# Performance work log

Measured on AMD Instinct MI355X. Metric: run time of the kernel, lower is better.

Reference implementation:

```python
import jax, jax.numpy as jnp
import numpy as np


def setup_inputs() -> dict:
    key = jax.random.key(0)
    k1, k2, k3, k4 = jax.random.split(key, 4)
    TOKENS, IN_F, OUT_F = 4096, 4096, 11008
    x = jax.random.normal(k1, (TOKENS, IN_F), dtype=jnp.float32)
    # int8-valued weights stored in fp32 buffer, as in the torch module
    quantized_weight = jax.random.randint(k2, (OUT_F, IN_F), -128, 128).astype(jnp.float32)
    # per-output-channel scales, positive, small (like max|w|/127)
    weight_scales = (jax.random.uniform(k3, (OUT_F, 1), dtype=jnp.float32) * 0.03 + 0.001)
    bias = jax.random.normal(k4, (OUT_F,), dtype=jnp.float32)
    return {"x": x, "quantized_weight": quantized_weight,
            "weight_scales": weight_scales, "bias": bias}


def reference(x, quantized_weight, weight_scales, bias):
    # dequantize: per-channel scale broadcast over in_features
    weight = quantized_weight * weight_scales  # [out, in]
    # F.linear: x @ weight.T + bias
    return jnp.dot(x, weight.T) + bias
```

## Files before the change

### kernel.cpp

```cpp
#include <hip/hip_runtime.h>
#include <hip/hip_bf16.h>


typedef __attribute__((ext_vector_type(4))) int   i32x4;
typedef __attribute__((ext_vector_type(4))) float f32x4;
typedef __attribute__((ext_vector_type(4))) unsigned int u32x4;

__device__ static inline unsigned int pack4(int q0, int q1, int q2, int q3) {
    return (unsigned)(q0 & 255) | ((unsigned)(q1 & 255) << 8) |
           ((unsigned)(q2 & 255) << 16) | ((unsigned)(q3 & 255) << 24);
}

__global__ void w_to_i8(const float* __restrict__ in,
                        u32x4* __restrict__ out, long n16) {
    const long stride = (long)gridDim.x * blockDim.x;
    for (long i = (long)blockIdx.x * blockDim.x + threadIdx.x; i < n16; i += stride) {
        const f32x4* p = reinterpret_cast<const f32x4*>(in) + i * 4;
        u32x4 o;
#pragma unroll
        for (int v = 0; v < 4; ++v) {
            f32x4 f = p[v];
            o[v] = pack4(__float2int_rn(f[0]), __float2int_rn(f[1]),
                         __float2int_rn(f[2]), __float2int_rn(f[3]));
        }
        out[i] = o;
    }
}

__global__ void x_quant_i8(const float* __restrict__ x,
                           unsigned int* __restrict__ xq,
                           float* __restrict__ sx, int K) {
    const int row = blockIdx.x;
    const int tid = threadIdx.x;
    const float* xr = x + (size_t)row * K;
    float m = 0.f;
    for (int b = tid * 16; b < K; b += blockDim.x * 16) {
        const f32x4* p = (const f32x4*)(xr + b);
#pragma unroll
        for (int v = 0; v < 4; ++v) {
            f32x4 f = p[v];
            m = fmaxf(m, fmaxf(fmaxf(fabsf(f[0]), fabsf(f[1])),
                               fmaxf(fabsf(f[2]), fabsf(f[3]))));
        }
    }
#pragma unroll
    for (int off = 32; off; off >>= 1) m = fmaxf(m, __shfl_xor(m, off));
    __shared__ float red[8];
    if ((tid & 63) == 0) red[tid >> 6] = m;
    __syncthreads();
    const int nw = blockDim.x >> 6;
    m = red[0];
    for (int i = 1; i < nw; ++i) m = fmaxf(m, red[i]);
    const float inv = (m > 0.f) ? 127.0f / m : 0.f;
    if (tid == 0) sx[row] = m * (1.0f / 127.0f);
    for (int b = tid * 16; b < K; b += blockDim.x * 16) {
        const f32x4* p = (const f32x4*)(xr + b);
        u32x4 o;
#pragma unroll
        for (int v = 0; v < 4; ++v) {
            f32x4 f = p[v];
            int q0 = min(127, max(-127, __float2int_rn(f[0] * inv)));
            int q1 = min(127, max(-127, __float2int_rn(f[1] * inv)));
            int q2 = min(127, max(-127, __float2int_rn(f[2] * inv)));
            int q3 = min(127, max(-127, __float2int_rn(f[3] * inv)));
            o[v] = pack4(q0, q1, q2, q3);
        }
        *reinterpret_cast<u32x4*>((char*)xq + (size_t)row * K + b) = o;
    }
}


#define GLOAD16(src, dst) __builtin_amdgcn_global_load_lds( \
    (const __attribute__((address_space(1))) void*)(src),   \
    (__attribute__((address_space(3))) void*)(dst), 16, 0, 0)

#define FENCE() asm volatile("" ::: "memory")
#define BAR()  do { FENCE(); __builtin_amdgcn_s_barrier(); FENCE(); } while (0)
#define WAIT_VM(n) asm volatile("s_waitcnt vmcnt(" #n ")" ::: "memory")
#define WAIT_LGKM0() asm volatile("s_waitcnt lgkmcnt(0)" ::: "memory")
#define PACE_LGKM(n) asm volatile("s_waitcnt lgkmcnt(" #n ")" ::: "memory")
#define SCHED0() __builtin_amdgcn_sched_barrier(0)

__global__ __launch_bounds__(512, 2)
void qlinear_gemm_i8k128(const char* __restrict__ A,
                         const char* __restrict__ B,
                         const float* __restrict__ sx,
                         const float* __restrict__ scales,
                         const float* __restrict__ bias,
                         float* __restrict__ C,
                         int M, int N, int K, int nbx) {
    __shared__ __align__(128) char smem[131072];

    const int tid  = threadIdx.x;
    const int lane = tid & 63;
    const int wid  = tid >> 6;
    const int wr   = wid >> 2;
    const int wc   = wid & 3;

    const int nwg = gridDim.x;
    const int q = nwg >> 3, r = nwg & 7;
    const int xcd = blockIdx.x & 7, boff_ = blockIdx.x >> 3;
    const int swz = (xcd < r ? xcd * (q + 1) : r * (q + 1) + (xcd - r) * q) + boff_;
    const int bcol = swz % nbx;
    const int brow = swz / nbx;

    const char* Ag = A + (size_t)brow * 256 * K;
    const char* Bg = B + (size_t)bcol * 256 * K;

    size_t sA[2], sB[2];
#pragma unroll
    for (int g = 0; g < 2; ++g) {
        const int c = tid + g * 512, rl = c >> 3, j = c & 7;
        const int rowA = ((rl >> 6) << 7) + (rl & 63);
        const int rowB = ((rl >> 5) << 6) + (rl & 31);
        sA[g] = (size_t)rowA * K + ((j ^ (rl & 7)) << 4);
        sB[g] = (size_t)rowB * K + ((j ^ (rl & 7)) << 4);
    }
    const int ld0 = tid * 16;

    auto stageA = [&](int rg, int h, int t) {
        const char* G = Ag + (size_t)h * 64 * K + (size_t)t * 128;
        char* base = smem + rg * 32768 + h * 16384;
        GLOAD16(G + sA[0], base + ld0);
        GLOAD16(G + sA[1], base + ld0 + 8192);
    };
    auto stageB = [&](int rg, int h, int t) {
        const char* G = Bg + (size_t)h * 32 * K + (size_t)t * 128;
        char* base = smem + 65536 + rg * 32768 + h * 16384;
        GLOAD16(G + sB[0], base + ld0);
        GLOAD16(G + sB[1], base + ld0 + 8192);
    };

    const int px0 = (((lane >> 4) ^ (lane & 7)) << 4);
    const int px1 = (((4 + (lane >> 4)) ^ (lane & 7)) << 4);
    const int arow = (wr * 64 + (lane & 15)) * 128;
    const int brw  = (wc * 32 + (lane & 15)) * 128;

    i32x4 acc[8][4] = {};
    i32x4 a0[8], a1[8], b0[4], b1[4];

    auto rdA = [&](int rg, int mh, i32x4 (&d)[8]) {
        const char* p = smem + rg * 32768 + mh * 16384 + arow;
#pragma unroll
        for (int i = 0; i < 4; ++i) {
            d[i * 2]     = *(const i32x4*)(p + i * 2048 + px0);
            d[i * 2 + 1] = *(const i32x4*)(p + i * 2048 + px1);
        }
    };
    auto rdB = [&](int rg, int nh, i32x4 (&d)[4]) {
        const char* p = smem + 65536 + rg * 32768 + nh * 16384 + brw;
#pragma unroll
        for (int n = 0; n < 2; ++n) {
            d[n * 2]     = *(const i32x4*)(p + n * 2048 + px0);
            d[n * 2 + 1] = *(const i32x4*)(p + n * 2048 + px1);
        }
    };
    auto mfma16 = [&](const i32x4 (&a)[8], const i32x4 (&b)[4], int mh, int nh) {
        __builtin_amdgcn_s_setprio(1);
#pragma unroll
        for (int i = 0; i < 4; ++i)
#pragma unroll
            for (int n = 0; n < 2; ++n) {
                i32x4& ac = acc[mh * 4 + i][nh * 2 + n];
                ac = __builtin_amdgcn_mfma_i32_16x16x64_i8(a[i * 2], b[n * 2], ac, 0, 0, 0);
                ac = __builtin_amdgcn_mfma_i32_16x16x64_i8(a[i * 2 + 1], b[n * 2 + 1], ac, 0, 0, 0);
            }
        __builtin_amdgcn_s_setprio(0);
    };

    const int NT = K / 128;

    stageA(0, 0, 0); stageB(0, 0, 0); stageA(0, 1, 0); stageB(0, 1, 0);
    stageA(1, 0, 1); stageB(1, 0, 1); stageA(1, 1, 1);
    WAIT_VM(6); BAR();

    for (int t = 0; t < NT - 2; ++t) {
        const int c = t & 1, o = c ^ 1;
        rdA(c, 0, a0); rdB(c, 0, b0);
        stageB(o, 1, t + 1);
        PACE_LGKM(8);
        BAR(); WAIT_LGKM0(); SCHED0();
        mfma16(a0, b0, 0, 0);
        BAR();
        rdA(c, 1, a1);
        stageA(c, 0, t + 2);
        BAR(); WAIT_LGKM0(); SCHED0();
        mfma16(a1, b0, 1, 0);
        BAR();
        rdB(c, 1, b1);
        stageB(c, 0, t + 2);
        BAR(); WAIT_LGKM0(); SCHED0();
        mfma16(a0, b1, 0, 1);
        BAR();
        stageA(c, 1, t + 2);
        mfma16(a1, b1, 1, 1);
        WAIT_VM(6);
        BAR();
    }
    {
        const int c = (NT - 2) & 1, o = c ^ 1;
        rdA(c, 0, a0); rdB(c, 0, b0);
        stageB(o, 1, NT - 1);
        PACE_LGKM(8);
        BAR(); WAIT_LGKM0(); SCHED0();
        mfma16(a0, b0, 0, 0);
        BAR();
        rdA(c, 1, a1);
        BAR(); WAIT_LGKM0(); SCHED0();
        mfma16(a1, b0, 1, 0);
        BAR();
        rdB(c, 1, b1);
        BAR(); WAIT_LGKM0(); SCHED0();
        mfma16(a0, b1, 0, 1);
        BAR();
        mfma16(a1, b1, 1, 1);
        WAIT_VM(0);
        BAR();
    }
    {
        const int c = (NT - 1) & 1;
        rdA(c, 0, a0); rdB(c, 0, b0);
        WAIT_LGKM0(); SCHED0();
        mfma16(a0, b0, 0, 0);
        rdA(c, 1, a1);
        WAIT_LGKM0(); SCHED0();
        mfma16(a1, b0, 1, 0);
        rdB(c, 1, b1);
        WAIT_LGKM0(); SCHED0();
        mfma16(a0, b1, 0, 1);
        mfma16(a1, b1, 1, 1);
    }

    const int lc  = lane & 15;
    const int lr4 = (lane >> 4) * 4;
    float sarr[4], barr[4];
#pragma unroll
    for (int ni = 0; ni < 4; ++ni) {
        const int n = bcol * 256 + wc * 64 + (ni >> 1) * 32 + (ni & 1) * 16 + lc;
        sarr[ni] = scales[n];
        barr[ni] = bias[n];
    }
#pragma unroll
    for (int mi = 0; mi < 8; ++mi) {
        const int mb = brow * 256 + wr * 128 + (mi >> 2) * 64 + (mi & 3) * 16 + lr4;
#pragma unroll
        for (int j = 0; j < 4; ++j) {
            const size_t rowoff = (size_t)(mb + j) * N;
            const float sm = sx[mb + j];
#pragma unroll
            for (int ni = 0; ni < 4; ++ni) {
                const int n = bcol * 256 + wc * 64 + (ni >> 1) * 32 + (ni & 1) * 16 + lc;
                C[rowoff + n] = fmaf((float)acc[mi][ni][j], sm * sarr[ni], barr[ni]);
            }
        }
    }
}

__global__ void qlinear_fallback(const float* __restrict__ A,
                                 const float* __restrict__ B,
                                 const float* __restrict__ scales,
                                 const float* __restrict__ bias,
                                 float* __restrict__ C, int M, int N, int K) {
    __shared__ float As[16][17], Bs[16][17];
    const int tx = threadIdx.x, ty = threadIdx.y;
    const int row = blockIdx.y * 16 + ty;
    const int col = blockIdx.x * 16 + tx;
    float acc = 0.f;
    for (int k0 = 0; k0 < K; k0 += 16) {
        As[ty][tx] = A[(long)row * K + k0 + tx];
        Bs[ty][tx] = B[(long)(blockIdx.x * 16 + ty) * K + k0 + tx];
        __syncthreads();
#pragma unroll
        for (int kk = 0; kk < 16; ++kk) acc += As[ty][kk] * Bs[tx][kk];
        __syncthreads();
    }
    C[(long)row * N + col] = fmaf(acc, scales[col], bias[col]);
}

extern "C" void kernel_launch(void* const* d_in, const int* in_sizes, int n_in,
                              void* d_out, int out_size, void* d_ws, size_t ws_size,
                              hipStream_t stream) {
    const float* x      = (const float*)d_in[0];
    const float* w      = (const float*)d_in[1];
    const float* scales = (const float*)d_in[2];
    const float* bias   = (const float*)d_in[3];
    float* out = (float*)d_out;

    const int N = in_sizes[2];
    const int K = (int)((long)in_sizes[1] / N);
    const int M = (int)((long)in_sizes[0] / K);

    const size_t need = (size_t)M * K + (size_t)N * K + (size_t)M * 4;
    const bool ok = (ws_size >= need) && (M % 256) == 0 && (N % 256) == 0 &&
                    (K % 128) == 0 && (K / 128) >= 3 && (K % 16) == 0;

    if (ok) {
        char* xq = (char*)d_ws;
        char* wq = xq + (size_t)M * K;
        float* sxbuf = (float*)(wq + (size_t)N * K);

        x_quant_i8<<<M, 256, 0, stream>>>(x, (unsigned int*)xq, sxbuf, K);
        w_to_i8<<<2048, 256, 0, stream>>>(w, (u32x4*)wq, (long)N * K / 16);

        const int nbx = N / 256;
        const int nwg = (M / 256) * nbx;
        qlinear_gemm_i8k128<<<nwg, 512, 0, stream>>>(xq, wq, sxbuf, scales, bias,
                                                     out, M, N, K, nbx);
    } else {
        dim3 grid(N / 16, M / 16), blk(16, 16);
        qlinear_fallback<<<grid, blk, 0, stream>>>(x, w, scales, bias, out, M, N, K);
    }
}
```

Before: 253.8 us.

## Restructure int8 GEMM main loop into two phases with fewer barriers

Reorganizes the K-loop from four barrier-separated MFMA quarters into two halves. Each half loads both B fragments (or the second A fragment) and issues two MFMA groups back-to-back. Global-to-LDS staging of the next tiles is regrouped so that A and B halves are issued together, and the prologue/wait counts are adjusted to match. This cuts barrier count per iteration and lengthens uninterrupted MFMA runs, at the cost of holding more fragment registers live at once. It also changes how far ahead prefetches are issued, which risks exposing load latency or LDS hazards.

```diff
diff --git a/kernel.cpp b/kernel.cpp
--- a/kernel.cpp
+++ b/kernel.cpp
@@ -78,17 +78,16 @@
 #define BAR()  do { FENCE(); __builtin_amdgcn_s_barrier(); FENCE(); } while (0)
 #define WAIT_VM(n) asm volatile("s_waitcnt vmcnt(" #n ")" ::: "memory")
 #define WAIT_LGKM0() asm volatile("s_waitcnt lgkmcnt(0)" ::: "memory")
-#define PACE_LGKM(n) asm volatile("s_waitcnt lgkmcnt(" #n ")" ::: "memory")
 #define SCHED0() __builtin_amdgcn_sched_barrier(0)
 
 __global__ __launch_bounds__(512, 2)
-void qlinear_gemm_i8k128(const char* __restrict__ A,
-                         const char* __restrict__ B,
-                         const float* __restrict__ sx,
-                         const float* __restrict__ scales,
-                         const float* __restrict__ bias,
-                         float* __restrict__ C,
-                         int M, int N, int K, int nbx) {
+void qlinear_gemm_i8v2(const char* __restrict__ A,
+                       const char* __restrict__ B,
+                       const float* __restrict__ sx,
+                       const float* __restrict__ scales,
+                       const float* __restrict__ bias,
+                       float* __restrict__ C,
+                       int M, int N, int K, int nbx) {
     __shared__ __align__(128) char smem[131072];
 
     const int tid  = threadIdx.x;
@@ -156,7 +155,6 @@
         }
     };
     auto mfma16 = [&](const i32x4 (&a)[8], const i32x4 (&b)[4], int mh, int nh) {
-        __builtin_amdgcn_s_setprio(1);
 #pragma unroll
         for (int i = 0; i < 4; ++i)
 #pragma unroll
@@ -165,69 +163,62 @@
                 ac = __builtin_amdgcn_mfma_i32_16x16x64_i8(a[i * 2], b[n * 2], ac, 0, 0, 0);
                 ac = __builtin_amdgcn_mfma_i32_16x16x64_i8(a[i * 2 + 1], b[n * 2 + 1], ac, 0, 0, 0);
             }
-        __builtin_amdgcn_s_setprio(0);
     };
 
     const int NT = K / 128;
 
     stageA(0, 0, 0); stageB(0, 0, 0); stageA(0, 1, 0); stageB(0, 1, 0);
-    stageA(1, 0, 1); stageB(1, 0, 1); stageA(1, 1, 1);
-    WAIT_VM(6); BAR();
+    stageA(1, 0, 1); stageB(1, 0, 1);
+    WAIT_VM(4); BAR();
 
     for (int t = 0; t < NT - 2; ++t) {
         const int c = t & 1, o = c ^ 1;
-        rdA(c, 0, a0); rdB(c, 0, b0);
-        stageB(o, 1, t + 1);
-        PACE_LGKM(8);
-        BAR(); WAIT_LGKM0(); SCHED0();
+        stageA(o, 1, t + 1); stageB(o, 1, t + 1);
+        rdA(c, 0, a0); rdB(c, 0, b0); rdB(c, 1, b1);
+        WAIT_LGKM0(); SCHED0();
+        __builtin_amdgcn_s_setprio(1);
         mfma16(a0, b0, 0, 0);
+        mfma16(a0, b1, 0, 1);
+        __builtin_amdgcn_s_setprio(0);
+        BAR();
+        stageA(c, 0, t + 2); stageB(c, 0, t + 2);
+        rdA(c, 1, a1);
+        WAIT_LGKM0(); SCHED0();
+        __builtin_amdgcn_s_setprio(1);
+        mfma16(a1, b0, 1, 0);
+        mfma16(a1, b1, 1, 1);
+        __builtin_amdgcn_s_setprio(0);
+        WAIT_VM(4);
+        BAR();
+    }
+    {
+        const int c = (NT - 2) & 1, o = c ^ 1;
+        stageA(o, 1, NT - 1); stageB(o, 1, NT - 1);
+        rdA(c, 0, a0); rdB(c, 0, b0); rdB(c, 1, b1);
+        WAIT_LGKM0(); SCHED0();
+        __builtin_amdgcn_s_setprio(1);
+        mfma16(a0, b0, 0, 0);
+        mfma16(a0, b1, 0, 1);
+        __builtin_amdgcn_s_setprio(0);
         BAR();
         rdA(c, 1, a1);
-        stageA(c, 0, t + 2);
-        BAR(); WAIT_LGKM0(); SCHED0();
+        WAIT_LGKM0(); SCHED0();
+        __builtin_amdgcn_s_setprio(1);
         mfma16(a1, b0, 1, 0);
-        BAR();
-        rdB(c, 1, b1);
-        stageB(c, 0, t + 2);
-        BAR(); WAIT_LGKM0(); SCHED0();
-        mfma16(a0, b1, 0, 1);
-        BAR();
-        stageA(c, 1, t + 2);
         mfma16(a1, b1, 1, 1);
-        WAIT_VM(6);
-        BAR();
-    }
-    {
-        const int c = (NT - 2) & 1, o = c ^ 1;
-        rdA(c, 0, a0); rdB(c, 0, b0);
-        stageB(o, 1, NT - 1);
-        PACE_LGKM(8);
-        BAR(); WAIT_LGKM0(); SCHED0();
-        mfma16(a0, b0, 0, 0);
-        BAR();
-        rdA(c, 1, a1);
-        BAR(); WAIT_LGKM0(); SCHED0();
-        mfma16(a1, b0, 1, 0);
-        BAR();
-        rdB(c, 1, b1);
-        BAR(); WAIT_LGKM0(); SCHED0();
-        mfma16(a0, b1, 0, 1);
-        BAR();
-        mfma16(a1, b1, 1, 1);
+        __builtin_amdgcn_s_setprio(0);
         WAIT_VM(0);
         BAR();
     }
     {
         const int c = (NT - 1) & 1;
-        rdA(c, 0, a0); rdB(c, 0, b0);
+        rdA(c, 0, a0); rdB(c, 0, b0); rdB(c, 1, b1);
         WAIT_LGKM0(); SCHED0();
         mfma16(a0, b0, 0, 0);
+        mfma16(a0, b1, 0, 1);
         rdA(c, 1, a1);
         WAIT_LGKM0(); SCHED0();
         mfma16(a1, b0, 1, 0);
-        rdB(c, 1, b1);
-        WAIT_LGKM0(); SCHED0();
-        mfma16(a0, b1, 0, 1);
         mfma16(a1, b1, 1, 1);
     }
 
@@ -304,8 +295,8 @@
 
         const int nbx = N / 256;
         const int nwg = (M / 256) * nbx;
-        qlinear_gemm_i8k128<<<nwg, 512, 0, stream>>>(xq, wq, sxbuf, scales, bias,
-                                                     out, M, N, K, nbx);
+        qlinear_gemm_i8v2<<<nwg, 512, 0, stream>>>(xq, wq, sxbuf, scales, bias,
+                                                   out, M, N, K, nbx);
     } else {
         dim3 grid(N / 16, M / 16), blk(16, 16);
         qlinear_fallback<<<grid, blk, 0, stream>>>(x, w, scales, bias, out, M, N, K);
```

New measurement: 254.8 us (median of 2 runs). About the same (+0.4%).
